# Kernel optimization log

Measured on AMD Instinct MI355X. Metric: run time of the kernel, lower is better.

## Reference

```python
import jax, jax.numpy as jnp
import numpy as np
from jax import lax


def _conv(x, w, b, pad, dil):
    # standard NCHW conv, OIHW weights
    y = lax.conv_general_dilated(x, w, (1, 1), [(pad, pad), (pad, pad)],
                                 rhs_dilation=(dil, dil),
                                 dimension_numbers=('NCHW', 'OIHW', 'NCHW'))
    return y + b[None, :, None, None]


def _bilinear(img, py, px):
    # img: [B,C,H,W]; py,px: [B,KK,H,W] float sample positions.
    # Zero-padding bilinear sampling (torchvision deform_conv semantics):
    # each of the 4 corners contributes 0 if it lies outside the image.
    B, C, H, W = img.shape
    y0 = jnp.floor(py)
    x0 = jnp.floor(px)
    wy1 = py - y0
    wx1 = px - x0
    imgf = img.reshape(B, C, H * W)

    def corner(yi, xi, wgt):
        valid = (yi >= 0) & (yi <= H - 1) & (xi >= 0) & (xi <= W - 1)
        yc = jnp.clip(yi, 0, H - 1).astype(jnp.int32)
        xc = jnp.clip(xi, 0, W - 1).astype(jnp.int32)
        idx = yc * W + xc  # [B,KK,H,W]
        g = jax.vmap(lambda im, ix: jnp.take(im, ix.reshape(-1), axis=1))(imgf, idx)
        g = g.reshape(B, C, *yi.shape[1:])  # [B,C,KK,H,W]
        return g * (wgt * valid.astype(img.dtype))[:, None]

    return (corner(y0, x0, (1 - wy1) * (1 - wx1))
            + corner(y0, x0 + 1, (1 - wy1) * wx1)
            + corner(y0 + 1, x0, wy1 * (1 - wx1))
            + corner(y0 + 1, x0 + 1, wy1 * wx1))


def _deform_dw(x, off_w, off_b, dw_w, K, pad, dil):
    # offset-predicted deformable depthwise conv (groups == channels)
    B, C, H, W = x.shape
    off = _conv(x, off_w, off_b, pad, dil).reshape(B, K * K, 2, H, W)
    dy, dx = off[:, :, 0], off[:, :, 1]  # torchvision order: (dy, dx) per tap
    ky, kx = jnp.meshgrid(jnp.arange(K), jnp.arange(K), indexing='ij')
    by = (ky.reshape(-1) * dil - pad).astype(x.dtype)  # [KK]
    bx = (kx.reshape(-1) * dil - pad).astype(x.dtype)
    py = jnp.arange(H, dtype=x.dtype)[None, None, :, None] + by[None, :, None, None] + dy
    px = jnp.arange(W, dtype=x.dtype)[None, None, None, :] + bx[None, :, None, None] + dx
    s = _bilinear(x, py, px)  # [B,C,KK,H,W]
    return jnp.einsum('bckhw,ck->bchw', s, dw_w.reshape(C, K * K))


def setup_inputs() -> dict:
    key = jax.random.key(0)
    ks = jax.random.split(key, 9)
    B, C, H, W = 4, 64, 56, 56
    f = lambda k, shape, s: jax.random.normal(k, shape, jnp.float32) * s
    return dict(
        x=f(ks[0], (B, C, H, W), 1.0),
        off_w1=f(ks[1], (2 * 5 * 5, C, 5, 5), 0.01), off_b1=f(ks[2], (2 * 5 * 5,), 0.01),
        dw_w1=f(ks[3], (C, 1, 5, 5), 0.1),
        off_w2=f(ks[4], (2 * 7 * 7, C, 7, 7), 0.01), off_b2=f(ks[5], (2 * 7 * 7,), 0.01),
        dw_w2=f(ks[6], (C, 1, 7, 7), 0.1),
        pw_w=f(ks[7], (C, C, 1, 1), 0.05), pw_b=f(ks[8], (C,), 0.05),
    )


def reference(x, off_w1, off_b1, dw_w1, off_w2, off_b2, dw_w2, pw_w, pw_b):
    attn = _deform_dw(x, off_w1, off_b1, dw_w1, 5, 2, 1)       # 5x5 deformable dw
    attn = _deform_dw(attn, off_w2, off_b2, dw_w2, 7, 9, 3)    # 7x7 dil-3 deformable dw
    attn = _conv(attn, pw_w, pw_b, 0, 1)                       # 1x1 pointwise
    return x * attn                                            # gated multiply
```

## Files before the change

kernel.cpp:

```cpp
#include <hip/hip_runtime.h>

#define BB 4
#define CC 64
#define HH 56
#define WW 56
#define HW (HH*WW)

typedef unsigned short u16;
typedef unsigned int u32;
typedef __attribute__((ext_vector_type(8))) short bf16x8;
typedef __attribute__((ext_vector_type(4))) float f32x4;

__device__ __forceinline__ u16 f2bf(float f) {
    union { float f; unsigned u; } c; c.f = f;
    unsigned u = c.u;
    u = (u + 0x7FFFu + ((u >> 16) & 1u)) >> 16;
    return (u16)u;
}
__device__ __forceinline__ float bf2f(u16 v) {
    union { unsigned u; float f; } c; c.u = ((unsigned)v) << 16;
    return c.f;
}
__device__ __forceinline__ float lo_f(u32 u) {
    union { unsigned u; float f; } c; c.u = u << 16; return c.f;
}
__device__ __forceinline__ float hi_f(u32 u) {
    union { unsigned u; float f; } c; c.u = u & 0xffff0000u; return c.f;
}

#define R1 102400
#define R2 401408
#define R3 4096
#define R4 1600
#define R5 3136
#define TGRID (BB*(HW/64))
#define PREPN (R1+R2+R3+R4+R5)
__global__ __launch_bounds__(256)
void prep_tr_kernel(const float* __restrict__ x,
                    const float* __restrict__ ow1, const float* __restrict__ ow2,
                    const float* __restrict__ pw,  const float* __restrict__ dw1,
                    const float* __restrict__ dw2,
                    u16* __restrict__ xT,
                    u16* __restrict__ w2t1, u16* __restrict__ w2t2,
                    u16* __restrict__ pwT, float* __restrict__ dwT1,
                    float* __restrict__ dwT2) {
    __shared__ u16 tile[64][72];
    const int t = threadIdx.x;
    if (blockIdx.x < TGRID) {
        const int blk = blockIdx.x;
        const int b   = blk / (HW/64);
        const int p0  = (blk % (HW/64))*64;
        const int px  = t & 63, icq = t >> 6;
        const float* ip = x + ((size_t)b*CC + icq*16)*HW + p0 + px;
        #pragma unroll
        for (int i = 0; i < 16; ++i)
            tile[px][icq*16 + i] = f2bf(ip[(size_t)i*HW]);
        __syncthreads();
        const int px2 = t >> 2, g = t & 3;
        u16* op = xT + ((size_t)b*HW + p0 + px2)*64 + g*16;
        const uint4* s = (const uint4*)&tile[px2][g*16];
        ((uint4*)op)[0] = s[0];
        ((uint4*)op)[1] = s[1];
        return;
    }
    const int i = (blockIdx.x - TGRID)*256 + t;
    if (i < R1) {
        const int ic = i & 63, n = (i >> 6) & 63, tap = i >> 12;
        w2t1[i] = f2bf((n < 50) ? ow1[((size_t)n*64 + ic)*25 + tap] : 0.f);
    } else if (i < R1+R2) {
        const int j = i - R1;
        const int ic = j & 63, n = (j >> 6) & 127, tap = j >> 13;
        w2t2[j] = f2bf((n < 98) ? ow2[((size_t)n*64 + ic)*49 + tap] : 0.f);
    } else if (i < R1+R2+R3) {
        const int j = i - (R1+R2);
        pwT[j] = f2bf(pw[j]);
    } else if (i < R1+R2+R3+R4) {
        const int j = i - (R1+R2+R3);
        const int c = j & 63, k = j >> 6;
        dwT1[j] = dw1[c*25 + k];
    } else if (i < R1+R2+R3+R4+R5) {
        const int j = i - (R1+R2+R3+R4);
        const int c = j & 63, k = j >> 6;
        dwT2[j] = dw2[c*49 + k];
    }
}

__device__ __forceinline__ uint4 selz(bool v, uint4 a) {
    const uint4 z = make_uint4(0,0,0,0);
    return v ? a : z;
}

template<int K, int DIL, int PAD, int COUT, int NP, int NPAD, int NTW>
__global__ __launch_bounds__(256, 4)
void conv_mfma_lds_kernel(const u16* __restrict__ xT, const u16* __restrict__ w2t,
                          const float* __restrict__ bias, float* __restrict__ out) {
    constexpr int KK = K*K;
    constexpr int BROWS = 16*NTW;
    __shared__ u16 Ab[2][64*64];
    __shared__ u16 Bb[2][BROWS*64];

    const int nm   = HW/64;
    const int b    = blockIdx.x / nm;
    const int p0   = (blockIdx.x % nm)*64;
    const int nt0  = blockIdx.y;
    const int t    = threadIdx.x;
    const int wave = t >> 6;
    const int lane = t & 63;

    const int spx = t >> 3;
    const int sc  = t & 7;
    const int pA  = p0 + spx;
    const int pB  = p0 + spx + 32;
    const int pyA = pA / WW, pxA = pA % WW;
    const int pyB = pB / WW, pxB = pB % WW;
    const u16* xb = xT + (size_t)b*HW*64;
    const int sslotA = ((sc + spx) & 7)*8;
    const int bn  = t >> 3;
    const int bslot = ((sc + bn) & 7)*8;
    const u16* wbase = w2t + (size_t)nt0*BROWS*64;

    const int r = lane & 15, quad = lane >> 4;
    const int mloc = wave*16 + r;
    const int arow = mloc*64;
    const int a0s = ((quad     + mloc) & 7)*8;
    const int a1s = ((quad + 4 + mloc) & 7)*8;
    const int b0s = ((quad     + r) & 7)*8;
    const int b1s = ((quad + 4 + r) & 7)*8;

    f32x4 acc[NTW];
    #pragma unroll
    for (int h = 0; h < NTW; ++h) acc[h] = (f32x4){0.f,0.f,0.f,0.f};
    const uint4 z4 = make_uint4(0,0,0,0);

    auto LD = [&](int tap, uint4& a0, uint4& a1, bool& va, bool& vb, uint4& bb) {
        const int dyy = (tap/K)*DIL - PAD;
        const int dxx = (tap%K)*DIL - PAD;
        const int off = dyy*WW + dxx;
        {
            const int yy = pyA + dyy, xx = pxA + dxx;
            va = ((unsigned)yy < (unsigned)HH) && ((unsigned)xx < (unsigned)WW);
            a0 = *(const uint4*)(xb + (size_t)(va ? (pA + off) : 0)*64 + sc*8);
        }
        {
            const int yy = pyB + dyy, xx = pxB + dxx;
            vb = ((unsigned)yy < (unsigned)HH) && ((unsigned)xx < (unsigned)WW);
            a1 = *(const uint4*)(xb + (size_t)(vb ? (pB + off) : 0)*64 + sc*8);
        }
        if (BROWS == 32 || bn < BROWS)
            bb = *(const uint4*)(wbase + ((size_t)tap*NP + bn)*64 + sc*8);
    };

    uint4 rA0 = z4, rA1 = z4, rB = z4;
    bool v0 = false, v1 = false;
    LD(0, rA0, rA1, v0, v1, rB);

    #pragma unroll
    for (int tap = 0; tap < KK; ++tap) {
        uint4 nA0 = z4, nA1 = z4, nB = z4;
        bool nv0 = false, nv1 = false;
        if (tap + 1 < KK) LD(tap + 1, nA0, nA1, nv0, nv1, nB);

        u16* A  = &Ab[tap & 1][0];
        u16* Bq = &Bb[tap & 1][0];
        *(uint4*)(A + spx*64      + sslotA) = selz(v0, rA0);
        *(uint4*)(A + (spx+32)*64 + sslotA) = selz(v1, rA1);
        if (BROWS == 32 || bn < BROWS) *(uint4*)(Bq + bn*64 + bslot) = rB;
        __syncthreads();

        const bf16x8 av0 = *(const bf16x8*)(A + arow + a0s);
        const bf16x8 av1 = *(const bf16x8*)(A + arow + a1s);
        #pragma unroll
        for (int h = 0; h < NTW; ++h) {
            const int brow = (h*16 + r)*64;
            const bf16x8 bv0 = *(const bf16x8*)(Bq + brow + b0s);
            const bf16x8 bv1 = *(const bf16x8*)(Bq + brow + b1s);
            acc[h] = __builtin_amdgcn_mfma_f32_16x16x32_bf16(av0, bv0, acc[h], 0, 0, 0);
            acc[h] = __builtin_amdgcn_mfma_f32_16x16x32_bf16(av1, bv1, acc[h], 0, 0, 0);
        }

        rA0 = nA0; rA1 = nA1; rB = nB; v0 = nv0; v1 = nv1;
    }

    #pragma unroll
    for (int h = 0; h < NTW; ++h) {
        const int n = nt0*BROWS + h*16 + r;
        if (n < COUT) {
            const float bv = bias[n];
            float* op = out + ((size_t)b*HW + p0 + wave*16 + quad*4)*NPAD + n;
            #pragma unroll
            for (int r2 = 0; r2 < 4; ++r2) op[(size_t)r2*NPAD] = acc[h][r2] + bv;
        }
    }
}

template<int K, int DIL, int PAD, int NPAD>
__global__ __launch_bounds__(256)
void deform_cl_kernel(const u16* __restrict__ inT, const float* __restrict__ offT,
                      const float* __restrict__ dwT, u16* __restrict__ outT) {
    constexpr int KK = K*K;
    __shared__ float4 swt[8][KK];
    __shared__ int4   sat[8][KK];
    __shared__ float  sdw[KK*64];

    const int t = threadIdx.x;
    const int nb8 = (BB*HW/8) >> 3;
    const int blk0 = blockIdx.x;
    const int blk = (blk0 & 7)*nb8 + (blk0 >> 3);
    const int p0 = blk*8;
    const int b  = p0 / HW;
    const int pl0 = p0 - b*HW;

    for (int i = t; i < KK*64; i += 256) sdw[i] = dwT[i];

    for (int i = t; i < 8*KK; i += 256) {
        const int pix = i / KK, k = i - pix*KK;
        const int pl  = pl0 + pix;
        const int h = pl / WW, w = pl % WW;
        const float* orow = offT + ((size_t)b*HW + pl)*NPAD;
        const float dy = orow[2*k];
        const float dx = orow[2*k+1];
        const float py = (float)(h + (k/K)*DIL - PAD) + dy;
        const float px = (float)(w + (k%K)*DIL - PAD) + dx;
        const float y0f = floorf(py), x0f = floorf(px);
        const float wy1 = py - y0f,  wx1 = px - x0f;
        const float wy0 = 1.f - wy1, wx0 = 1.f - wx1;
        const int y0 = (int)y0f, x0 = (int)x0f;

        const int y0c = min(max(y0,   0), HH-1);
        const int y1c = min(max(y0+1, 0), HH-1);
        const int x0c = min(max(x0,   0), WW-1);
        const int x1c = min(max(x0+1, 0), WW-1);
        const float gy0 = wy0 * ((y0   >= 0 && y0   < HH) ? 1.f : 0.f);
        const float gy1 = wy1 * ((y0+1 >= 0 && y0+1 < HH) ? 1.f : 0.f);
        const float gx0 = wx0 * ((x0   >= 0 && x0   < WW) ? 1.f : 0.f);
        const float gx1 = wx1 * ((x0+1 >= 0 && x0+1 < WW) ? 1.f : 0.f);

        swt[pix][k] = make_float4(gy0*gx0, gy0*gx1, gy1*gx0, gy1*gx1);
        const int r0 = y0c*WW, r1 = y1c*WW;
        sat[pix][k] = make_int4((r0 + x0c) << 7, (r0 + x1c) << 7,
                                (r1 + x0c) << 7, (r1 + x1c) << 7);
    }
    __syncthreads();

    const int wave = t >> 6, lane = t & 63;
    const int pixl = 2*wave + (lane >> 5);
    const int chp  = lane & 31;
    const char* ib = (const char*)(inT + (size_t)b*HW*64) + chp*4;

    float accx = 0.f, accy = 0.f;
    #pragma unroll 7
    for (int k = 0; k < KK; ++k) {
        const float4 wv = swt[pixl][k];
        const int4   av = sat[pixl][k];
        const u32 c00 = *(const u32*)(ib + av.x);
        const u32 c01 = *(const u32*)(ib + av.y);
        const u32 c10 = *(const u32*)(ib + av.z);
        const u32 c11 = *(const u32*)(ib + av.w);
        const float sx = lo_f(c00)*wv.x + lo_f(c01)*wv.y + lo_f(c10)*wv.z + lo_f(c11)*wv.w;
        const float sy = hi_f(c00)*wv.x + hi_f(c01)*wv.y + hi_f(c10)*wv.z + hi_f(c11)*wv.w;
        const float2 dw2 = *(const float2*)&sdw[k*64 + 2*chp];
        accx += sx * dw2.x;
        accy += sy * dw2.y;
    }
    const u32 o = (u32)f2bf(accx) | ((u32)f2bf(accy) << 16);
    *(u32*)((char*)outT + (size_t)(p0 + pixl)*128 + chp*4) = o;
}

__global__ __launch_bounds__(256)
void pw_mfma_kernel(const u16* __restrict__ a2T, const u16* __restrict__ pwT,
                    const float* __restrict__ pb, const float* __restrict__ x,
                    float* __restrict__ out) {
    const int nm = HW/64;
    const int b  = blockIdx.x / nm;
    const int p0 = (blockIdx.x % nm)*64 + (threadIdx.x >> 6)*16;
    const int nt = blockIdx.y;
    const int lane = threadIdx.x & 63;
    const int r = lane & 15, quad = lane >> 4;

    const u16* ap = a2T + ((size_t)b*HW + p0 + r)*64 + quad*8;
    f32x4 acc = (f32x4){0.f,0.f,0.f,0.f};
    #pragma unroll
    for (int ks = 0; ks < 2; ++ks) {
        const bf16x8 av = *(const bf16x8*)(ap + ks*32);
        const bf16x8 bv = *(const bf16x8*)(pwT + ((size_t)(nt*16 + r))*64 + ks*32 + quad*8);
        acc = __builtin_amdgcn_mfma_f32_16x16x32_bf16(av, bv, acc, 0, 0, 0);
    }

    const int n = nt*16 + r;
    const float bv = pb[n];
    const size_t base = ((size_t)b*CC + n)*HW + p0 + quad*4;
    #pragma unroll
    for (int r2 = 0; r2 < 4; ++r2)
        out[base + r2] = x[base + r2] * (acc[r2] + bv);
}

template<int K, int DIL, int PAD, int COUT, int OCB>
__global__ __launch_bounds__(256)
void off_conv_sg_kernel(const float* __restrict__ in, const float* __restrict__ wgt,
                        const float* __restrict__ bias, float* __restrict__ out) {
    constexpr int KK = K*K;
    const int nOB = COUT / OCB;
    const int b   = blockIdx.x / nOB;
    const int oc0 = (blockIdx.x % nOB) * OCB;
    const int x   = threadIdx.x;
    const int h   = blockIdx.y*4 + threadIdx.y;

    float acc[OCB];
    #pragma unroll
    for (int o = 0; o < OCB; ++o) acc[o] = bias[oc0+o];

    const float* inb = in + (size_t)b*CC*HW;
    const float* wb  = wgt + (size_t)oc0*CC*KK;

    for (int ic = 0; ic < CC; ++ic) {
        const float* inp = inb + ic*HW;
        const float* wp  = wb + ic*KK;
        #pragma unroll
        for (int ky = 0; ky < K; ++ky) {
            const int  y  = h + ky*DIL - PAD;
            const bool yv = (y >= 0) && (y < HH);
            const int  yc = yv ? y : 0;
            const float* row = inp + yc*WW;
            #pragma unroll
            for (int kx = 0; kx < K; ++kx) {
                const int  xx = x + kx*DIL - PAD;
                const bool v  = yv && (xx >= 0) && (xx < WW);
                const int  xc = (xx < 0) ? 0 : ((xx >= WW) ? (WW-1) : xx);
                float val = row[xc];
                val = v ? val : 0.f;
                const int t = ky*K + kx;
                #pragma unroll
                for (int o = 0; o < OCB; ++o)
                    acc[o] += wp[(size_t)o*CC*KK + t] * val;
            }
        }
    }

    if (x >= WW) return;
    #pragma unroll
    for (int o = 0; o < OCB; ++o)
        out[((size_t)b*COUT + oc0 + o)*HW + h*WW + x] = acc[o];
}

template<int K, int DIL, int PAD>
__global__ __launch_bounds__(64)
void deform_dw_full_kernel(const float* __restrict__ in, const float* __restrict__ off,
                           const float* __restrict__ dw, float* __restrict__ out) {
    constexpr int KK = K*K;
    const int idx = blockIdx.x*64 + threadIdx.x;
    const int x = idx % WW;
    const int h = (idx / WW) % HH;
    const int c = (idx / HW) % CC;
    const int b = idx / (CC*HW);

    const float* inp  = in  + ((size_t)b*CC + c)*HW;
    const float* offp = off + (size_t)b*(2*KK)*HW + h*WW + x;
    const float* dwp  = dw  + c*KK;

    float acc = 0.f;
    #pragma unroll 7
    for (int k = 0; k < KK; ++k) {
        const float dy = offp[(2*k  )*HW];
        const float dx = offp[(2*k+1)*HW];
        const float py = (float)(h + (k/K)*DIL - PAD) + dy;
        const float px = (float)(x + (k%K)*DIL - PAD) + dx;
        const float y0f = floorf(py), x0f = floorf(px);
        const float wy1 = py - y0f,  wx1 = px - x0f;
        const float wy0 = 1.f - wy1, wx0 = 1.f - wx1;
        const int y0 = (int)y0f, x0 = (int)x0f;

        const int y0c = min(max(y0,   0), HH-1);
        const int y1c = min(max(y0+1, 0), HH-1);
        const int x0c = min(max(x0,   0), WW-1);
        const int x1c = min(max(x0+1, 0), WW-1);
        const float my0 = (y0   >= 0 && y0   < HH) ? 1.f : 0.f;
        const float my1 = (y0+1 >= 0 && y0+1 < HH) ? 1.f : 0.f;
        const float mx0 = (x0   >= 0 && x0   < WW) ? 1.f : 0.f;
        const float mx1 = (x0+1 >= 0 && x0+1 < WW) ? 1.f : 0.f;

        const float v00 = inp[y0c*WW + x0c];
        const float v01 = inp[y0c*WW + x1c];
        const float v10 = inp[y1c*WW + x0c];
        const float v11 = inp[y1c*WW + x1c];

        const float gx0 = wx0*mx0, gx1 = wx1*mx1;
        const float s = (v00*gx0 + v01*gx1) * (wy0*my0)
                      + (v10*gx0 + v11*gx1) * (wy1*my1);
        acc += s * dwp[k];
    }
    out[idx] = acc;
}

__global__ __launch_bounds__(256)
void pw_mul_kernel(const float* __restrict__ x, const float* __restrict__ a2,
                   const float* __restrict__ pw, const float* __restrict__ pb,
                   float* __restrict__ out) {
    constexpr int HW4 = HW/4;
    const int t = blockIdx.x*256 + threadIdx.x;
    if (t >= BB*CC*HW4) return;
    const int sp4 = t % HW4;
    const int oc  = (t / HW4) % CC;
    const int b   = t / (CC*HW4);

    const float4* ap = (const float4*)(a2 + (size_t)b*CC*HW) + sp4;
    const float4* wp4 = (const float4*)(pw + oc*CC);
    const float pbv = pb[oc];
    float4 acc = make_float4(pbv, pbv, pbv, pbv);
    #pragma unroll 4
    for (int ic4 = 0; ic4 < CC/4; ++ic4) {
        const float4 w = wp4[ic4];
        float4 a0 = ap[(ic4*4+0)*HW4];
        float4 a1 = ap[(ic4*4+1)*HW4];
        float4 a2v = ap[(ic4*4+2)*HW4];
        float4 a3 = ap[(ic4*4+3)*HW4];
        acc.x += w.x*a0.x + w.y*a1.x + w.z*a2v.x + w.w*a3.x;
        acc.y += w.x*a0.y + w.y*a1.y + w.z*a2v.y + w.w*a3.y;
        acc.z += w.x*a0.z + w.y*a1.z + w.z*a2v.z + w.w*a3.z;
        acc.w += w.x*a0.w + w.y*a1.w + w.z*a2v.w + w.w*a3.w;
    }
    const float4 xv = ((const float4*)x)[t];
    float4 r;
    r.x = xv.x*acc.x; r.y = xv.y*acc.y; r.z = xv.z*acc.z; r.w = xv.w*acc.w;
    ((float4*)out)[t] = r;
}

extern "C" void kernel_launch(void* const* d_in, const int* in_sizes, int n_in,
                              void* d_out, int out_size, void* d_ws, size_t ws_size,
                              hipStream_t stream) {
    const float* x      = (const float*)d_in[0];
    const float* off_w1 = (const float*)d_in[1];
    const float* off_b1 = (const float*)d_in[2];
    const float* dw_w1  = (const float*)d_in[3];
    const float* off_w2 = (const float*)d_in[4];
    const float* off_b2 = (const float*)d_in[5];
    const float* dw_w2  = (const float*)d_in[6];
    const float* pw_w   = (const float*)d_in[7];
    const float* pw_b   = (const float*)d_in[8];
    float* out = (float*)d_out;

    const size_t nF    = (size_t)BB*CC*HW;
    const size_t attnB = nF*sizeof(float);
    const size_t off2B = (size_t)BB*98*HW*sizeof(float);
    const size_t offTB = (size_t)BB*HW*112*sizeof(float);
    const size_t chB   = (size_t)BB*HW*64*sizeof(u16);
    char* ws = (char*)d_ws;

    const int n    = (int)nF;
    const int dbl  = n/64;
    const int pbl  = (n/4 + 255)/256;
    dim3 cblk(64,4);
    dim3 rgrd1(BB*(50/5), HH/4);
    dim3 rgrd2(BB*(98/7), HH/4);
    dim3 cgrd1(TGRID, 2);
    dim3 cgrd2(TGRID, 4);
    dim3 pgrd(TGRID, 4);
    const int dgrid = BB*HW/8;

    const size_t oOFF  = 0;
    const size_t oXT   = oOFF + offTB;
    const size_t oA1T  = oXT  + chB;
    const size_t oA2T  = oA1T + chB;
    const size_t oW1   = oA2T + chB;
    const size_t oW2   = oW1  + (size_t)R1*2;
    const size_t oPWT  = oW2  + (size_t)R2*2;
    const size_t oDW1  = oPWT + (size_t)R3*2;
    const size_t oDW2  = oDW1 + (size_t)R4*4;
    const size_t TOT   = oDW2 + (size_t)R5*4;

    if (ws_size >= TOT) {
        float* off_buf = (float*)(ws + oOFF);
        u16*   xT      = (u16*)(ws + oXT);
        u16*   a1T     = (u16*)(ws + oA1T);
        u16*   a2T     = (u16*)(ws + oA2T);
        u16*   w2t1    = (u16*)(ws + oW1);
        u16*   w2t2    = (u16*)(ws + oW2);
        u16*   pwT     = (u16*)(ws + oPWT);
        float* dwT1    = (float*)(ws + oDW1);
        float* dwT2    = (float*)(ws + oDW2);

        prep_tr_kernel<<<TGRID + (PREPN+255)/256, 256, 0, stream>>>(
            x, off_w1, off_w2, pw_w, dw_w1, dw_w2,
            xT, w2t1, w2t2, pwT, dwT1, dwT2);

        conv_mfma_lds_kernel<5,1,2,50,64,64,2><<<cgrd1, 256, 0, stream>>>(xT, w2t1, off_b1, off_buf);
        deform_cl_kernel<5,1,2,64><<<dgrid, 256, 0, stream>>>(xT, off_buf, dwT1, a1T);

        conv_mfma_lds_kernel<7,3,9,98,128,112,2><<<cgrd2, 256, 0, stream>>>(a1T, w2t2, off_b2, off_buf);
        deform_cl_kernel<7,3,9,112><<<dgrid, 256, 0, stream>>>(a1T, off_buf, dwT2, a2T);

        pw_mfma_kernel<<<pgrd, 256, 0, stream>>>(a2T, pwT, pw_b, x, out);
    } else if (ws_size >= off2B + attnB) {
        float* off_buf = (float*)ws;
        float* attn1   = (float*)d_out;
        float* attn2   = (float*)(ws + off2B);
        off_conv_sg_kernel<5,1,2,50,5><<<rgrd1, cblk, 0, stream>>>(x, off_w1, off_b1, off_buf);
        deform_dw_full_kernel<5,1,2><<<dbl, 64, 0, stream>>>(x, off_buf, dw_w1, attn1);
        off_conv_sg_kernel<7,3,9,98,7><<<rgrd2, cblk, 0, stream>>>(attn1, off_w2, off_b2, off_buf);
        deform_dw_full_kernel<7,3,9><<<dbl, 64, 0, stream>>>(attn1, off_buf, dw_w2, attn2);
        pw_mul_kernel<<<pbl, 256, 0, stream>>>(x, attn2, pw_w, pw_b, out);
    } else {
        float* attn1 = (float*)d_out;
        float* attn2 = (float*)ws;
        float* off1  = (float*)ws;
        off_conv_sg_kernel<5,1,2,50,5><<<rgrd1, cblk, 0, stream>>>(x, off_w1, off_b1, off1);
        deform_dw_full_kernel<5,1,2><<<dbl, 64, 0, stream>>>(x, off1, dw_w1, attn1);
        float* off2 = (float*)(ws + attnB);
        off_conv_sg_kernel<7,3,9,98,7><<<rgrd2, cblk, 0, stream>>>(attn1, off_w2, off_b2, off2);
        deform_dw_full_kernel<7,3,9><<<dbl, 64, 0, stream>>>(attn1, off2, dw_w2, attn2);
        pw_mul_kernel<<<pbl, 256, 0, stream>>>(x, attn2, pw_w, pw_b, out);
    }
}
```

Measured before the change: 158.6 us.

## Vectorize deformable gather to 16-byte loads and skip padded offset-conv tiles

The deformable depthwise kernel now has each thread handle 8 channels of one pixel using 16-byte gathers per bilinear corner, instead of 2 channels with 4-byte loads. Blocks shrink to 128 threads covering 16 pixels, which cuts the number of memory instructions per sample but raises per-thread register use. The offset conv gains an NREAL parameter to skip weight loads and MFMAs for N-tiles wholly beyond the real output count, so the second conv drops its fully padded tile (112..127). This should reduce wasted tensor work in the 7x7 offset conv.

```diff
diff --git a/kernel.cpp b/kernel.cpp
--- a/kernel.cpp
+++ b/kernel.cpp
@@ -90,7 +90,7 @@
     return v ? a : z;
 }
 
-template<int K, int DIL, int PAD, int COUT, int NP, int NPAD, int NTW>
+template<int K, int DIL, int PAD, int COUT, int NP, int NPAD, int NTW, int NREAL>
 __global__ __launch_bounds__(256, 4)
 void conv_mfma_lds_kernel(const u16* __restrict__ xT, const u16* __restrict__ w2t,
                           const float* __restrict__ bias, float* __restrict__ out) {
@@ -118,6 +118,7 @@
     const int bn  = t >> 3;
     const int bslot = ((sc + bn) & 7)*8;
     const u16* wbase = w2t + (size_t)nt0*BROWS*64;
+    const bool bactive = (BROWS == 32 || bn < BROWS) && (nt0*BROWS + bn < NREAL);
 
     const int r = lane & 15, quad = lane >> 4;
     const int mloc = wave*16 + r;
@@ -146,7 +147,7 @@
             vb = ((unsigned)yy < (unsigned)HH) && ((unsigned)xx < (unsigned)WW);
             a1 = *(const uint4*)(xb + (size_t)(vb ? (pB + off) : 0)*64 + sc*8);
         }
-        if (BROWS == 32 || bn < BROWS)
+        if (bactive)
             bb = *(const uint4*)(wbase + ((size_t)tap*NP + bn)*64 + sc*8);
     };
 
@@ -164,13 +165,14 @@
         u16* Bq = &Bb[tap & 1][0];
         *(uint4*)(A + spx*64      + sslotA) = selz(v0, rA0);
         *(uint4*)(A + (spx+32)*64 + sslotA) = selz(v1, rA1);
-        if (BROWS == 32 || bn < BROWS) *(uint4*)(Bq + bn*64 + bslot) = rB;
+        if (bactive) *(uint4*)(Bq + bn*64 + bslot) = rB;
         __syncthreads();
 
         const bf16x8 av0 = *(const bf16x8*)(A + arow + a0s);
         const bf16x8 av1 = *(const bf16x8*)(A + arow + a1s);
         #pragma unroll
         for (int h = 0; h < NTW; ++h) {
+            if (NREAL < NP && nt0*BROWS + h*16 >= NREAL) break;
             const int brow = (h*16 + r)*64;
             const bf16x8 bv0 = *(const bf16x8*)(Bq + brow + b0s);
             const bf16x8 bv1 = *(const bf16x8*)(Bq + brow + b1s);
@@ -194,25 +196,26 @@
 }
 
 template<int K, int DIL, int PAD, int NPAD>
-__global__ __launch_bounds__(256)
+__global__ __launch_bounds__(128)
 void deform_cl_kernel(const u16* __restrict__ inT, const float* __restrict__ offT,
                       const float* __restrict__ dwT, u16* __restrict__ outT) {
     constexpr int KK = K*K;
-    __shared__ float4 swt[8][KK];
-    __shared__ int4   sat[8][KK];
+    constexpr int PXB = 16;
+    __shared__ float4 swt[PXB][KK];
+    __shared__ int4   sat[PXB][KK];
     __shared__ float  sdw[KK*64];
 
     const int t = threadIdx.x;
-    const int nb8 = (BB*HW/8) >> 3;
+    const int nbX = (BB*HW/PXB) >> 3;
     const int blk0 = blockIdx.x;
-    const int blk = (blk0 & 7)*nb8 + (blk0 >> 3);
-    const int p0 = blk*8;
+    const int blk = (blk0 & 7)*nbX + (blk0 >> 3);
+    const int p0 = blk*PXB;
     const int b  = p0 / HW;
     const int pl0 = p0 - b*HW;
 
-    for (int i = t; i < KK*64; i += 256) sdw[i] = dwT[i];
-
-    for (int i = t; i < 8*KK; i += 256) {
+    for (int i = t; i < KK*64; i += 128) sdw[i] = dwT[i];
+
+    for (int i = t; i < PXB*KK; i += 128) {
         const int pix = i / KK, k = i - pix*KK;
         const int pl  = pl0 + pix;
         const int h = pl / WW, w = pl % WW;
@@ -242,28 +245,46 @@
     }
     __syncthreads();
 
-    const int wave = t >> 6, lane = t & 63;
-    const int pixl = 2*wave + (lane >> 5);
-    const int chp  = lane & 31;
-    const char* ib = (const char*)(inT + (size_t)b*HW*64) + chp*4;
-
-    float accx = 0.f, accy = 0.f;
-    #pragma unroll 7
+    const int lane = t & 63, wave = t >> 6;
+    const int pix  = wave*8 + (lane >> 3);
+    const int cq   = lane & 7;
+    const char* ib = (const char*)(inT + (size_t)b*HW*64) + cq*16;
+
+    float acc[8];
+    #pragma unroll
+    for (int j = 0; j < 8; ++j) acc[j] = 0.f;
+
+    #pragma unroll 4
     for (int k = 0; k < KK; ++k) {
-        const float4 wv = swt[pixl][k];
-        const int4   av = sat[pixl][k];
-        const u32 c00 = *(const u32*)(ib + av.x);
-        const u32 c01 = *(const u32*)(ib + av.y);
-        const u32 c10 = *(const u32*)(ib + av.z);
-        const u32 c11 = *(const u32*)(ib + av.w);
-        const float sx = lo_f(c00)*wv.x + lo_f(c01)*wv.y + lo_f(c10)*wv.z + lo_f(c11)*wv.w;
-        const float sy = hi_f(c00)*wv.x + hi_f(c01)*wv.y + hi_f(c10)*wv.z + hi_f(c11)*wv.w;
-        const float2 dw2 = *(const float2*)&sdw[k*64 + 2*chp];
-        accx += sx * dw2.x;
-        accy += sy * dw2.y;
-    }
-    const u32 o = (u32)f2bf(accx) | ((u32)f2bf(accy) << 16);
-    *(u32*)((char*)outT + (size_t)(p0 + pixl)*128 + chp*4) = o;
+        const float4 wv = swt[pix][k];
+        const int4   av = sat[pix][k];
+        const uint4 c00 = *(const uint4*)(ib + av.x);
+        const uint4 c01 = *(const uint4*)(ib + av.y);
+        const uint4 c10 = *(const uint4*)(ib + av.z);
+        const uint4 c11 = *(const uint4*)(ib + av.w);
+        const float4 d0 = *(const float4*)&sdw[k*64 + cq*8];
+        const float4 d1 = *(const float4*)&sdw[k*64 + cq*8 + 4];
+        const float dv[8] = {d0.x,d0.y,d0.z,d0.w,d1.x,d1.y,d1.z,d1.w};
+        const u32* p00 = (const u32*)&c00;
+        const u32* p01 = (const u32*)&c01;
+        const u32* p10 = (const u32*)&c10;
+        const u32* p11 = (const u32*)&c11;
+        #pragma unroll
+        for (int j = 0; j < 4; ++j) {
+            const u32 u00 = p00[j], u01 = p01[j], u10 = p10[j], u11 = p11[j];
+            const float slo = lo_f(u00)*wv.x + lo_f(u01)*wv.y + lo_f(u10)*wv.z + lo_f(u11)*wv.w;
+            const float shi = hi_f(u00)*wv.x + hi_f(u01)*wv.y + hi_f(u10)*wv.z + hi_f(u11)*wv.w;
+            acc[2*j]   += slo * dv[2*j];
+            acc[2*j+1] += shi * dv[2*j+1];
+        }
+    }
+
+    uint4 ov;
+    u32* ow = (u32*)&ov;
+    #pragma unroll
+    for (int j = 0; j < 4; ++j)
+        ow[j] = (u32)f2bf(acc[2*j]) | ((u32)f2bf(acc[2*j+1]) << 16);
+    *(uint4*)((char*)outT + (size_t)(p0 + pix)*128 + cq*16) = ov;
 }
 
 __global__ __launch_bounds__(256)
@@ -454,7 +475,7 @@
     dim3 cgrd1(TGRID, 2);
     dim3 cgrd2(TGRID, 4);
     dim3 pgrd(TGRID, 4);
-    const int dgrid = BB*HW/8;
+    const int dgrid = BB*HW/16;
 
     const size_t oOFF  = 0;
     const size_t oXT   = oOFF + offTB;
@@ -482,11 +503,11 @@
             x, off_w1, off_w2, pw_w, dw_w1, dw_w2,
             xT, w2t1, w2t2, pwT, dwT1, dwT2);
 
-        conv_mfma_lds_kernel<5,1,2,50,64,64,2><<<cgrd1, 256, 0, stream>>>(xT, w2t1, off_b1, off_buf);
-        deform_cl_kernel<5,1,2,64><<<dgrid, 256, 0, stream>>>(xT, off_buf, dwT1, a1T);
-
-        conv_mfma_lds_kernel<7,3,9,98,128,112,2><<<cgrd2, 256, 0, stream>>>(a1T, w2t2, off_b2, off_buf);
-        deform_cl_kernel<7,3,9,112><<<dgrid, 256, 0, stream>>>(a1T, off_buf, dwT2, a2T);
+        conv_mfma_lds_kernel<5,1,2,50,64,64,2,64><<<cgrd1, 256, 0, stream>>>(xT, w2t1, off_b1, off_buf);
+        deform_cl_kernel<5,1,2,64><<<dgrid, 128, 0, stream>>>(xT, off_buf, dwT1, a1T);
+
+        conv_mfma_lds_kernel<7,3,9,98,128,112,2,112><<<cgrd2, 256, 0, stream>>>(a1T, w2t2, off_b2, off_buf);
+        deform_cl_kernel<7,3,9,112><<<dgrid, 128, 0, stream>>>(a1T, off_buf, dwT2, a2T);
 
         pw_mfma_kernel<<<pgrd, 256, 0, stream>>>(a2T, pwT, pw_b, x, out);
     } else if (ws_size >= off2B + attnB) {
```

Result: slower. 165.1 us (+4.1%).
